# Kernel tuning notes

Measured on AMD Instinct MI355X. Metric: run time of the kernel, lower is better.

Reference implementation:

```python
import jax, jax.numpy as jnp
import numpy as np

B, M, D = 16, 16, 512          # m (tokens per sample) must equal num_experts
N = 16                          # num_experts
H = (D + D) * 2 // 3            # hidden_dim = 682
OUT = 512


def setup_inputs() -> dict:
    key = jax.random.key(0)
    ks = jax.random.split(key, 8)
    s = lambda k, shape, fan: jax.random.normal(k, shape, jnp.float32) / np.sqrt(fan)
    return {
        "x":    jax.random.normal(ks[0], (B, M, D), jnp.float32),
        "phi":  jax.random.normal(ks[1], (D, N, H), jnp.float32),
        "W1":   s(ks[2], (N, D, H), D),
        "b1":   s(ks[3], (N, H), D),
        "W2":   s(ks[4], (N, H, D), H),
        "b2":   s(ks[5], (N, D), H),
        "Wout": s(ks[6], (N * D, OUT), N * D),
        "bout": s(ks[7], (OUT,), N * D),
    }


def reference(x, phi, W1, b1, W2, b2, Wout, bout):
    # dispatch/combine logits: [b, m, n, p]
    logits = jnp.einsum('bmd,dnp->bmnp', x, phi)
    Dw = jax.nn.softmax(logits, axis=1)                       # dispatch weights over tokens m
    Cw = jax.nn.softmax(jax.nn.softmax(logits, axis=2), axis=3)  # (softmax of softmax, faithful)
    Xs = jnp.einsum('bmd,bmnp->bnpd', x, Dw)                  # expert slot inputs [b,n,p,d]
    # batched per-expert MLP (grouped GEMM over expert axis n)
    hmid = jax.nn.relu(jnp.einsum('bnpd,ndh->bnph', Xs, W1) + b1[None, :, None, :])
    Ys = jnp.einsum('bnph,nhd->bnpd', hmid, W2) + b2[None, :, None, :]
    Y = jnp.einsum('bnpd,bmnp->bmd', Ys, Cw)                  # combine -> [b, m, d]
    flat = Y.reshape(Y.shape[0], -1)                          # [b, m*d] == [b, n*d]
    return flat @ Wout + bout
```

## Files before the change

### kernel.cpp

```cpp
#include <hip/hip_runtime.h>
#include <hip/hip_bf16.h>
#include <math.h>

typedef unsigned int   u32;
typedef unsigned short u16;
typedef __bf16 bf16;
typedef bf16  bf16x8  __attribute__((ext_vector_type(8)));
typedef float f32x4   __attribute__((ext_vector_type(4)));
typedef float f32x16  __attribute__((ext_vector_type(16)));

#define BBATCH 16
#define MTOK   16
#define NEXP   16
#define DDIM   512
#define HDIM   682
#define HPAD   704
#define NHCOL  (NEXP*HDIM)
#define NHPCOL (NEXP*HPAD)

__device__ __forceinline__ u16 f2bf(float f) {
    u32 u = __builtin_bit_cast(u32, f);
    u += 0x7fffu + ((u >> 16) & 1u);
    return (u16)(u >> 16);
}
__device__ __forceinline__ float bf2f(u16 h) {
    u32 u = ((u32)h) << 16;
    return __builtin_bit_cast(float, u);
}
__device__ __forceinline__ u32 pk2bf(float a, float b) {
    __hip_bfloat162 t = __float22bfloat162_rn(float2{a, b});
    u32 r;
    __builtin_memcpy(&r, &t, 4);
    return r;
}

__global__ __launch_bounds__(256) void k_prep(
    const float* __restrict__ x,
    u16* __restrict__ xh, u16* __restrict__ xl) {
    const int bid = blockIdx.x, tid = threadIdx.x;
    int i = (bid * 256 + tid) * 4;
    float4 v = *(const float4*)&x[i];
    float a[4] = {v.x, v.y, v.z, v.w};
    u16 hh[4], ll[4];
    #pragma unroll
    for (int j = 0; j < 4; ++j) {
        hh[j] = f2bf(a[j]);
        ll[j] = f2bf(a[j] - bf2f(hh[j]));
    }
    *(uint2*)&xh[i] = make_uint2((u32)hh[0] | ((u32)hh[1] << 16), (u32)hh[2] | ((u32)hh[3] << 16));
    *(uint2*)&xl[i] = make_uint2((u32)ll[0] | ((u32)ll[1] << 16), (u32)ll[2] | ((u32)ll[3] << 16));
}

__global__ __launch_bounds__(256) void k_lt1(
    const u16* __restrict__ xh, const u16* __restrict__ xl,
    const float* __restrict__ phi, const float* __restrict__ W1,
    float* __restrict__ logits, u16* __restrict__ DwT, u16* __restrict__ T1b) {
    __shared__ __align__(16) char SMEM[29184];
    const int bid = blockIdx.x, tid = threadIdx.x;
    const int wv = tid >> 6, lane = tid & 63, quad = lane >> 4, l15 = lane & 15;
    if (bid < 704) {
        const int xcd = bid & 7, slot = bid >> 3;
        const int rt = slot & 3, ct = (slot >> 2) * 8 + xcd;
        if (ct >= 171) {
            const int hole = (slot & 3) * 5 + (xcd - 3);
            for (int g = hole * 256 + tid; g < 22528; g += 5120) {
                int bn = g / 88, off = g - bn * 88;
                *(uint2*)(DwT + (size_t)(bn * HPAD + HDIM) * 16 + off * 4) =
                    make_uint2(0u, 0u);
            }
            return;
        }
        u16* AH = (u16*)SMEM;
        u16* AL = (u16*)(SMEM + 5120);
        u16* BH = (u16*)(SMEM + 10240);
        u16* BL = (u16*)(SMEM + 15360);
        float* F = (float*)(SMEM + 20480);
        const int r = tid >> 2, kg = (tid & 3) * 8;
        const u16* aph = xh + (size_t)(rt * 64 + r) * 512 + kg;
        const u16* apl = xl + (size_t)(rt * 64 + r) * 512 + kg;
        const int dl = tid >> 3, cg = (tid & 7) * 8;
        const int c0 = ct * 64 + cg;
        float vB[8];
        auto loadB = [&](int kb) {
            const float* src = phi + (size_t)(kb + dl) * NHCOL + c0;
            if (c0 + 8 <= NHCOL) {
                *(float4*)&vB[0] = *(const float4*)&src[0];
                *(float4*)&vB[4] = *(const float4*)&src[4];
            } else {
                #pragma unroll
                for (int i = 0; i < 8; ++i) vB[i] = (c0 + i < NHCOL) ? src[i] : 0.f;
            }
        };
        uint4 rAh = *(const uint4*)aph;
        uint4 rAl = *(const uint4*)apl;
        loadB(0);
        f32x4 acc[4] = {};
        for (int kb = 0; kb < 512; kb += 32) {
            *(uint4*)&AH[r * 40 + kg] = rAh;
            *(uint4*)&AL[r * 40 + kg] = rAl;
            *(float4*)&F[dl * 68 + cg]     = *(float4*)&vB[0];
            *(float4*)&F[dl * 68 + cg + 4] = *(float4*)&vB[4];
            __syncthreads();
            if (kb + 32 < 512) {
                rAh = *(const uint4*)(aph + kb + 32);
                rAl = *(const uint4*)(apl + kb + 32);
                loadB(kb + 32);
            }
            {
                int cc = tid & 63, q = tid >> 6;
                u16 th[8], tl[8];
                #pragma unroll
                for (int i = 0; i < 8; ++i) {
                    float v = F[(q * 8 + i) * 68 + cc];
                    th[i] = f2bf(v);
                    tl[i] = f2bf(v - bf2f(th[i]));
                }
                *(uint4*)&BH[cc * 40 + q * 8] = *(uint4*)&th[0];
                *(uint4*)&BL[cc * 40 + q * 8] = *(uint4*)&tl[0];
            }
            __syncthreads();
            bf16x8 ah = *(const bf16x8*)&AH[(wv * 16 + l15) * 40 + quad * 8];
            bf16x8 al = *(const bf16x8*)&AL[(wv * 16 + l15) * 40 + quad * 8];
            #pragma unroll
            for (int j = 0; j < 4; ++j) {
                bf16x8 bh = *(const bf16x8*)&BH[(j * 16 + l15) * 40 + quad * 8];
                bf16x8 bl = *(const bf16x8*)&BL[(j * 16 + l15) * 40 + quad * 8];
                acc[j] = __builtin_amdgcn_mfma_f32_16x16x32_bf16(ah, bh, acc[j], 0, 0, 0);
                acc[j] = __builtin_amdgcn_mfma_f32_16x16x32_bf16(ah, bl, acc[j], 0, 0, 0);
                acc[j] = __builtin_amdgcn_mfma_f32_16x16x32_bf16(al, bh, acc[j], 0, 0, 0);
            }
            __syncthreads();
        }
        const int b  = rt * 4 + wv;
        const int r0 = rt * 64 + wv * 16 + quad * 4;
        #pragma unroll
        for (int j = 0; j < 4; ++j) {
            const int col = ct * 64 + j * 16 + l15;
            float a0 = acc[j][0], a1 = acc[j][1], a2 = acc[j][2], a3 = acc[j][3];
            if (col < NHCOL) {
                logits[(size_t)(r0 + 0) * NHCOL + col] = a0;
                logits[(size_t)(r0 + 1) * NHCOL + col] = a1;
                logits[(size_t)(r0 + 2) * NHCOL + col] = a2;
                logits[(size_t)(r0 + 3) * NHCOL + col] = a3;
            }
            float mx = fmaxf(fmaxf(a0, a1), fmaxf(a2, a3));
            mx = fmaxf(mx, __shfl_xor(mx, 16));
            mx = fmaxf(mx, __shfl_xor(mx, 32));
            float e0 = expf(a0 - mx), e1 = expf(a1 - mx);
            float e2 = expf(a2 - mx), e3 = expf(a3 - mx);
            float s = e0 + e1 + e2 + e3;
            s += __shfl_xor(s, 16);
            s += __shfl_xor(s, 32);
            float inv = 1.f / s;
            if (col < NHCOL) {
                int n = col / HDIM;
                int p2 = col - n * HDIM;
                u16* dst = DwT + ((size_t)((b * 16 + n) * HPAD + p2)) * 16 + quad * 4;
                *(uint2*)dst = make_uint2(pk2bf(e0 * inv, e1 * inv), pk2bf(e2 * inv, e3 * inv));
            }
        }
    } else {
        const int b2_ = bid - 704;
        const int xcd = b2_ & 7, slot = b2_ >> 3;
        const int rh = slot & 1, ct = (slot >> 1) * 8 + xcd;
        const int n = ct / 11, h0 = (ct % 11) * 64;
        u16* As = (u16*)SMEM;
        u16* Bs = (u16*)(SMEM + 10240);
        float* F = (float*)(SMEM + 15360);
        const int r = tid >> 1, kg = (tid & 1) * 16;
        const u16* ap = xh + (size_t)(rh * 128 + r) * 512 + kg;
        const int dl = tid >> 3, cg = (tid & 7) * 8;
        const int h = h0 + cg;
        float vB[8];
        auto loadB = [&](int kb) {
            const float* wr = W1 + ((size_t)n * 512 + kb + dl) * HDIM + h;
            if (h + 8 <= HDIM) {
                #pragma unroll
                for (int i = 0; i < 4; ++i) {
                    float2 t = *(const float2*)&wr[i * 2];
                    vB[i * 2] = t.x; vB[i * 2 + 1] = t.y;
                }
            } else {
                #pragma unroll
                for (int i = 0; i < 8; ++i) vB[i] = (h + i < HDIM) ? wr[i] : 0.f;
            }
        };
        uint4 rA0 = *(const uint4*)ap;
        uint4 rA1 = *(const uint4*)(ap + 8);
        loadB(0);
        f32x4 acc[2][4] = {};
        for (int kb = 0; kb < 512; kb += 32) {
            *(uint4*)&As[r * 40 + kg]     = rA0;
            *(uint4*)&As[r * 40 + kg + 8] = rA1;
            *(float4*)&F[dl * 68 + cg]     = *(float4*)&vB[0];
            *(float4*)&F[dl * 68 + cg + 4] = *(float4*)&vB[4];
            __syncthreads();
            if (kb + 32 < 512) {
                rA0 = *(const uint4*)(ap + kb + 32);
                rA1 = *(const uint4*)(ap + kb + 40);
                loadB(kb + 32);
            }
            {
                int cc = tid & 63, q = tid >> 6;
                u16 tv[8];
                #pragma unroll
                for (int i = 0; i < 8; ++i) tv[i] = f2bf(F[(q * 8 + i) * 68 + cc]);
                *(uint4*)&Bs[cc * 40 + q * 8] = *(uint4*)&tv[0];
            }
            __syncthreads();
            bf16x8 af[2], bfr[4];
            #pragma unroll
            for (int i = 0; i < 2; ++i)
                af[i] = *(const bf16x8*)&As[(wv * 32 + i * 16 + l15) * 40 + quad * 8];
            #pragma unroll
            for (int j = 0; j < 4; ++j)
                bfr[j] = *(const bf16x8*)&Bs[(j * 16 + l15) * 40 + quad * 8];
            #pragma unroll
            for (int i = 0; i < 2; ++i)
                #pragma unroll
                for (int j = 0; j < 4; ++j)
                    acc[i][j] = __builtin_amdgcn_mfma_f32_16x16x32_bf16(af[i], bfr[j], acc[i][j], 0, 0, 0);
            __syncthreads();
        }
        #pragma unroll
        for (int i = 0; i < 2; ++i)
            #pragma unroll
            for (int j = 0; j < 4; ++j) {
                int col = ct * 64 + j * 16 + l15;
                int r0  = rh * 128 + wv * 32 + i * 16 + quad * 4;
                #pragma unroll
                for (int rr = 0; rr < 4; ++rr)
                    T1b[(size_t)(r0 + rr) * NHPCOL + col] = f2bf(acc[i][j][rr]);
            }
    }
}

__global__ __launch_bounds__(512) void k_cw(
    const float* __restrict__ L, u16* __restrict__ CwB,
    const float* __restrict__ b2, const float* __restrict__ bout,
    float* __restrict__ Y, float* __restrict__ out) {
    __shared__ __align__(16) float row[NHCOL];
    const int bid = blockIdx.x, tid = threadIdx.x;
    if (bid >= 256) {
        if (bid < 512) {
            int idx = (bid - 256) * 512 + tid;
            int d = idx & 511;
            float s = 0.f;
            #pragma unroll
            for (int nn = 0; nn < 16; ++nn) s += b2[nn * 512 + d];
            Y[idx] = s;
        } else {
            int idx = (bid - 512) * 512 + tid;
            out[idx] = bout[idx & 511];
        }
        return;
    }
    const int m = bid & 15, b = bid >> 4;
    const float* Lrow = L + (size_t)(b * 16 + m) * NHCOL;
    for (int i4 = tid; i4 < NHCOL / 4; i4 += 512)
        *(float4*)&row[i4 * 4] = *(const float4*)&Lrow[i4 * 4];
    __syncthreads();
    for (int p = tid; p < HDIM; p += 512) {
        float v[16];
        float mx = -1e30f;
        #pragma unroll
        for (int n = 0; n < 16; ++n) { v[n] = row[n * HDIM + p]; mx = fmaxf(mx, v[n]); }
        float s = 0.f;
        #pragma unroll
        for (int n = 0; n < 16; ++n) { v[n] = expf(v[n] - mx); s += v[n]; }
        float inv = 1.f / s;
        #pragma unroll
        for (int n = 0; n < 16; ++n) row[n * HDIM + p] = expf(v[n] * inv);
    }
    __syncthreads();
    const int wv = tid >> 6, lane = tid & 63;
    for (int nn = 0; nn < 2; ++nn) {
        int n = wv * 2 + nn;
        float s = 0.f;
        for (int p = lane; p < HDIM; p += 64) s += row[n * HDIM + p];
        #pragma unroll
        for (int off = 32; off > 0; off >>= 1) s += __shfl_xor(s, off);
        float inv = 1.f / s;
        u16* dst = CwB + (size_t)(((b * 16 + n) * 16 + m)) * HPAD;
        for (int p = lane; p < HDIM; p += 64) dst[p] = f2bf(row[n * HDIM + p] * inv);
        if (lane < HPAD - HDIM) dst[HDIM + lane] = 0;
    }
}

__global__ __launch_bounds__(256) void k_mid(
    const u16* __restrict__ T1b, const u16* __restrict__ DwT,
    const u16* __restrict__ CwB, const float* __restrict__ b1,
    u16* __restrict__ Gb) {
    __shared__ u16 T1T[128 * 24];
    __shared__ u16 hmidT[128 * 64];
    const int bid = blockIdx.x;
    const int xcd = bid & 7, slot = bid >> 3;
    const int ht = slot % 6, gg = slot / 6;
    const int g = gg * 8 + xcd;
    const int n = g & 15, b = g >> 4;
    const int tid = threadIdx.x;
    const int wv = tid >> 6, lane = tid & 63;
    const int quad = lane >> 4, l15 = lane & 15;
    const int l31 = lane & 31, half = lane >> 5;
    const int h0 = ht * 128;
    const int b16n = b * 16 + n;

    {
        int m = tid & 15, hh0 = (tid >> 4) * 8;
        u16 v[8];
        if (h0 + hh0 + 8 <= HPAD) {
            *(uint4*)v = *(const uint4*)(T1b + (size_t)(b * 16 + m) * NHPCOL + n * HPAD + h0 + hh0);
        } else {
            #pragma unroll
            for (int i = 0; i < 8; ++i) v[i] = 0;
        }
        #pragma unroll
        for (int i = 0; i < 8; ++i) T1T[(hh0 + i) * 24 + m] = v[i];
    }
    __syncthreads();

    const int hrow = wv * 32 + l31;
    bf16x8 bt1 = *(const bf16x8*)&T1T[hrow * 24 + half * 8];
    int hg1 = h0 + hrow;
    float biasf = (hg1 < HDIM) ? b1[n * HDIM + hg1] : 0.f;
    f32x16 cbias;
    #pragma unroll
    for (int i = 0; i < 16; ++i) cbias[i] = biasf;

    const u16* dwbase = DwT + (size_t)(b16n * HPAD) * 16;
    const u16* cwrow  = CwB + (size_t)(b16n * 16 + l15) * HPAD;

    f32x4 acc[2] = {};
    const int hsw = hrow & 7;
    for (int c = 0; c < 11; ++c) {
        const int p0 = c * 64;
        #pragma unroll
        for (int pt = 0; pt < 2; ++pt) {
            bf16x8 adw = *(const bf16x8*)(dwbase + (size_t)(p0 + pt * 32 + l31) * 16 + half * 8);
            f32x16 hm = __builtin_amdgcn_mfma_f32_32x32x16_bf16(adw, bt1, cbias, 0, 0, 0);
            #pragma unroll
            for (int g2 = 0; g2 < 4; ++g2) {
                float v0 = fmaxf(hm[g2 * 4 + 0], 0.f);
                float v1 = fmaxf(hm[g2 * 4 + 1], 0.f);
                float v2 = fmaxf(hm[g2 * 4 + 2], 0.f);
                float v3 = fmaxf(hm[g2 * 4 + 3], 0.f);
                uint2 pk = make_uint2(pk2bf(v0, v1), pk2bf(v2, v3));
                int gran = (pt * 4 + g2) ^ hsw;
                *(uint2*)&hmidT[hrow * 64 + gran * 8 + half * 4] = pk;
            }
        }
        #pragma unroll
        for (int s = 0; s < 2; ++s) {
            bf16x8 acw = *(const bf16x8*)(cwrow + p0 + s * 32 + quad * 8);
            #pragma unroll
            for (int hj = 0; hj < 2; ++hj) {
                int hr = wv * 32 + hj * 16 + l15;
                int gr = (s * 4 + quad) ^ (hr & 7);
                bf16x8 bh = *(const bf16x8*)&hmidT[hr * 64 + gr * 8];
                acc[hj] = __builtin_amdgcn_mfma_f32_16x16x32_bf16(acw, bh, acc[hj], 0, 0, 0);
            }
        }
    }
    #pragma unroll
    for (int hj = 0; hj < 2; ++hj) {
        int h = h0 + wv * 32 + hj * 16 + l15;
        if (h < HPAD) {
            #pragma unroll
            for (int r = 0; r < 4; ++r) {
                int m = quad * 4 + r;
                Gb[(size_t)(b * 16 + m) * NHPCOL + n * HPAD + h] = f2bf(acc[hj][r]);
            }
        }
    }
}

__global__ __launch_bounds__(256) void k_ygemm(
    const u16* __restrict__ G, const float* __restrict__ W2, float* __restrict__ Y) {
    __shared__ u16 AsL[64 * 40];
    __shared__ u16 BsL[128 * 40];
    __shared__ float F[32 * 132];
    const int bid = blockIdx.x;
    const int xcd = bid & 7, slot = bid >> 3;
    const int rt = slot & 3, gg = slot >> 2;
    const int g = gg * 8 + xcd;
    const int ct = g & 3, nz = g >> 2;
    const int n = nz >> 1, kb0 = (nz & 1) * 352;
    const int tid = threadIdx.x;
    const int wv = tid >> 6, lane = tid & 63, quad = lane >> 4, l15 = lane & 15;
    const int m0 = rt * 64, d0 = ct * 128;
    const int am = tid >> 2, akg = (tid & 3) * 8;
    const u16* apg = G + (size_t)(m0 + am) * NHPCOL + n * HPAD + akg;
    const int hl = tid >> 3, cg = (tid & 7) * 16;
    float vB[16];
    auto loadB = [&](int kb) {
        int h = kb + hl;
        if (h < HDIM) {
            const float* src = W2 + ((size_t)n * HDIM + h) * 512 + d0 + cg;
            *(float4*)&vB[0]  = *(const float4*)&src[0];
            *(float4*)&vB[4]  = *(const float4*)&src[4];
            *(float4*)&vB[8]  = *(const float4*)&src[8];
            *(float4*)&vB[12] = *(const float4*)&src[12];
        } else {
            #pragma unroll
            for (int i = 0; i < 16; ++i) vB[i] = 0.f;
        }
    };
    uint4 rA = *(const uint4*)(apg + kb0);
    loadB(kb0);
    f32x4 acc[4][2] = {};
    for (int kb = kb0; kb < kb0 + 352; kb += 32) {
        *(uint4*)&AsL[am * 40 + akg] = rA;
        *(float4*)&F[hl * 132 + cg]      = *(float4*)&vB[0];
        *(float4*)&F[hl * 132 + cg + 4]  = *(float4*)&vB[4];
        *(float4*)&F[hl * 132 + cg + 8]  = *(float4*)&vB[8];
        *(float4*)&F[hl * 132 + cg + 12] = *(float4*)&vB[12];
        __syncthreads();
        if (kb + 32 < kb0 + 352) {
            rA = *(const uint4*)(apg + kb + 32);
            loadB(kb + 32);
        }
        {
            int cc = tid & 127, half = tid >> 7;
            u16 tv[16];
            #pragma unroll
            for (int i = 0; i < 16; ++i) tv[i] = f2bf(F[(half * 16 + i) * 132 + cc]);
            *(uint4*)&BsL[cc * 40 + half * 16]     = *(uint4*)&tv[0];
            *(uint4*)&BsL[cc * 40 + half * 16 + 8] = *(uint4*)&tv[8];
        }
        __syncthreads();
        bf16x8 af[4], bfr[2];
        #pragma unroll
        for (int i = 0; i < 4; ++i) af[i] = *(const bf16x8*)&AsL[(i * 16 + l15) * 40 + quad * 8];
        #pragma unroll
        for (int j = 0; j < 2; ++j) bfr[j] = *(const bf16x8*)&BsL[(wv * 32 + j * 16 + l15) * 40 + quad * 8];
        #pragma unroll
        for (int i = 0; i < 4; ++i)
            #pragma unroll
            for (int j = 0; j < 2; ++j)
                acc[i][j] = __builtin_amdgcn_mfma_f32_16x16x32_bf16(af[i], bfr[j], acc[i][j], 0, 0, 0);
        __syncthreads();
    }
    #pragma unroll
    for (int i = 0; i < 4; ++i)
        #pragma unroll
        for (int j = 0; j < 2; ++j) {
            int dcol = d0 + wv * 32 + j * 16 + l15;
            int r0 = m0 + i * 16 + quad * 4;
            #pragma unroll
            for (int r = 0; r < 4; ++r)
                atomicAdd(&Y[(size_t)(r0 + r) * 512 + dcol], acc[i][j][r]);
        }
}

__global__ __launch_bounds__(256) void k_outgemm(
    const float* __restrict__ Y, const float* __restrict__ Wout, float* __restrict__ out) {
    __shared__ u16 AsL[16 * 40];
    __shared__ u16 BsL[128 * 40];
    __shared__ float F[32 * 132];
    const int ct = blockIdx.x, ks = blockIdx.y;
    const int tid = threadIdx.x;
    const int wv = tid >> 6, lane = tid & 63, quad = lane >> 4, l15 = lane & 15;
    const int o0 = ct * 128, kbase = ks * 64;
    f32x4 acc[2] = {};
    for (int kb = 0; kb < 64; kb += 32) {
        {
            int r = tid >> 4, k2 = (tid & 15) * 2;
            float2 v = *(const float2*)&Y[(size_t)r * 8192 + kbase + kb + k2];
            AsL[r * 40 + k2]     = f2bf(v.x);
            AsL[r * 40 + k2 + 1] = f2bf(v.y);
        }
        {
            int kl = tid >> 3, cg = (tid & 7) * 16;
            const float* src = Wout + (size_t)(kbase + kb + kl) * 512 + o0 + cg;
            float v[16];
            *(float4*)&v[0]  = *(const float4*)&src[0];
            *(float4*)&v[4]  = *(const float4*)&src[4];
            *(float4*)&v[8]  = *(const float4*)&src[8];
            *(float4*)&v[12] = *(const float4*)&src[12];
            #pragma unroll
            for (int i = 0; i < 16; ++i) F[kl * 132 + cg + i] = v[i];
        }
        __syncthreads();
        {
            int cc = tid & 127, half = tid >> 7;
            u16 tv[16];
            #pragma unroll
            for (int i = 0; i < 16; ++i) tv[i] = f2bf(F[(half * 16 + i) * 132 + cc]);
            *(uint4*)&BsL[cc * 40 + half * 16]     = *(uint4*)&tv[0];
            *(uint4*)&BsL[cc * 40 + half * 16 + 8] = *(uint4*)&tv[8];
        }
        __syncthreads();
        bf16x8 af = *(const bf16x8*)&AsL[l15 * 40 + quad * 8];
        #pragma unroll
        for (int j = 0; j < 2; ++j) {
            bf16x8 bfr = *(const bf16x8*)&BsL[(wv * 32 + j * 16 + l15) * 40 + quad * 8];
            acc[j] = __builtin_amdgcn_mfma_f32_16x16x32_bf16(af, bfr, acc[j], 0, 0, 0);
        }
        __syncthreads();
    }
    #pragma unroll
    for (int j = 0; j < 2; ++j) {
        int o = o0 + wv * 32 + j * 16 + l15;
        #pragma unroll
        for (int r = 0; r < 4; ++r)
            atomicAdd(&out[(size_t)(quad * 4 + r) * 512 + o], acc[j][r]);
    }
}

extern "C" void kernel_launch(void* const* d_in, const int* in_sizes, int n_in,
                              void* d_out, int out_size, void* d_ws, size_t ws_size,
                              hipStream_t stream) {
    const float* x    = (const float*)d_in[0];
    const float* phi  = (const float*)d_in[1];
    const float* W1   = (const float*)d_in[2];
    const float* b1   = (const float*)d_in[3];
    const float* W2   = (const float*)d_in[4];
    const float* b2   = (const float*)d_in[5];
    const float* Wout = (const float*)d_in[6];
    const float* bout = (const float*)d_in[7];
    float* out = (float*)d_out;

    char* base = (char*)d_ws;
    float* logits = (float*)(base + 0);
    u16*   DwT    = (u16*)(base + 11173888);
    u16*   CwB    = (u16*)(base + 16941056);
    u16*   T1b    = (u16*)(base + 22708224);
    u16*   Gb     = (u16*)(base + 28475392);
    u16*   xh     = (u16*)(base + 34242560);
    u16*   xl     = (u16*)(base + 34504704);
    float* Y      = (float*)(base + 34766848);

    k_prep    <<<dim3(128), 256, 0, stream>>>(x, xh, xl);
    k_lt1     <<<dim3(1056), 256, 0, stream>>>(xh, xl, phi, W1, logits, DwT, T1b);
    k_cw      <<<dim3(528), 512, 0, stream>>>(logits, CwB, b2, bout, Y, out);
    k_mid     <<<dim3(1536), 256, 0, stream>>>(T1b, DwT, CwB, b1, Gb);
    k_ygemm   <<<dim3(512), 256, 0, stream>>>(Gb, W2, Y);
    k_outgemm <<<dim3(4, 128), 256, 0, stream>>>(Y, Wout, out);
}
```

Measured before the change: 209.0 us.

## Fuse mid stage with W2 GEMM, accumulating Y directly via atomics

Merges k_mid and k_ygemm into one kernel: each block stages its G tile (16 tokens x 128 hidden) in shared memory and multiplies it by the matching W2 slice, atomically adding partial results into Y. The Gb intermediate buffer and one kernel launch are removed, and the block-to-expert mapping is changed so each XCD keeps a fixed expert, which may help L2 reuse of W2. The cost is that W2 is read with scalar, strided global loads converted to bf16 per element with no shared-memory staging. Each W2 row is also read by all 16 batch blocks, and there are many more atomics into Y.

```diff
diff --git a/kernel.cpp b/kernel.cpp
--- a/kernel.cpp
+++ b/kernel.cpp
@@ -287,17 +287,19 @@
     }
 }
 
-__global__ __launch_bounds__(256) void k_mid(
+__global__ __launch_bounds__(256) void k_midy(
     const u16* __restrict__ T1b, const u16* __restrict__ DwT,
     const u16* __restrict__ CwB, const float* __restrict__ b1,
-    u16* __restrict__ Gb) {
-    __shared__ u16 T1T[128 * 24];
-    __shared__ u16 hmidT[128 * 64];
+    const float* __restrict__ W2, float* __restrict__ Y) {
+    __shared__ __align__(16) char SMEM[22528];
+    u16* T1T   = (u16*)SMEM;
+    u16* hmidT = (u16*)(SMEM + 6144);
+    u16* GT    = (u16*)SMEM;
     const int bid = blockIdx.x;
     const int xcd = bid & 7, slot = bid >> 3;
-    const int ht = slot % 6, gg = slot / 6;
-    const int g = gg * 8 + xcd;
-    const int n = g & 15, b = g >> 4;
+    const int nhi = slot & 1, rem = slot >> 1;
+    const int ht = rem % 6, b = rem / 6;
+    const int n = nhi * 8 + xcd;
     const int tid = threadIdx.x;
     const int wv = tid >> 6, lane = tid & 63;
     const int quad = lane >> 4, l15 = lane & 15;
@@ -361,95 +363,43 @@
             }
         }
     }
+
+    __syncthreads();
     #pragma unroll
     for (int hj = 0; hj < 2; ++hj) {
-        int h = h0 + wv * 32 + hj * 16 + l15;
-        if (h < HPAD) {
-            #pragma unroll
-            for (int r = 0; r < 4; ++r) {
-                int m = quad * 4 + r;
-                Gb[(size_t)(b * 16 + m) * NHPCOL + n * HPAD + h] = f2bf(acc[hj][r]);
-            }
-        }
-    }
-}
-
-__global__ __launch_bounds__(256) void k_ygemm(
-    const u16* __restrict__ G, const float* __restrict__ W2, float* __restrict__ Y) {
-    __shared__ u16 AsL[64 * 40];
-    __shared__ u16 BsL[128 * 40];
-    __shared__ float F[32 * 132];
-    const int bid = blockIdx.x;
-    const int xcd = bid & 7, slot = bid >> 3;
-    const int rt = slot & 3, gg = slot >> 2;
-    const int g = gg * 8 + xcd;
-    const int ct = g & 3, nz = g >> 2;
-    const int n = nz >> 1, kb0 = (nz & 1) * 352;
-    const int tid = threadIdx.x;
-    const int wv = tid >> 6, lane = tid & 63, quad = lane >> 4, l15 = lane & 15;
-    const int m0 = rt * 64, d0 = ct * 128;
-    const int am = tid >> 2, akg = (tid & 3) * 8;
-    const u16* apg = G + (size_t)(m0 + am) * NHPCOL + n * HPAD + akg;
-    const int hl = tid >> 3, cg = (tid & 7) * 16;
-    float vB[16];
-    auto loadB = [&](int kb) {
-        int h = kb + hl;
-        if (h < HDIM) {
-            const float* src = W2 + ((size_t)n * HDIM + h) * 512 + d0 + cg;
-            *(float4*)&vB[0]  = *(const float4*)&src[0];
-            *(float4*)&vB[4]  = *(const float4*)&src[4];
-            *(float4*)&vB[8]  = *(const float4*)&src[8];
-            *(float4*)&vB[12] = *(const float4*)&src[12];
-        } else {
-            #pragma unroll
-            for (int i = 0; i < 16; ++i) vB[i] = 0.f;
-        }
-    };
-    uint4 rA = *(const uint4*)(apg + kb0);
-    loadB(kb0);
-    f32x4 acc[4][2] = {};
-    for (int kb = kb0; kb < kb0 + 352; kb += 32) {
-        *(uint4*)&AsL[am * 40 + akg] = rA;
-        *(float4*)&F[hl * 132 + cg]      = *(float4*)&vB[0];
-        *(float4*)&F[hl * 132 + cg + 4]  = *(float4*)&vB[4];
-        *(float4*)&F[hl * 132 + cg + 8]  = *(float4*)&vB[8];
-        *(float4*)&F[hl * 132 + cg + 12] = *(float4*)&vB[12];
-        __syncthreads();
-        if (kb + 32 < kb0 + 352) {
-            rA = *(const uint4*)(apg + kb + 32);
-            loadB(kb + 32);
-        }
-        {
-            int cc = tid & 127, half = tid >> 7;
-            u16 tv[16];
-            #pragma unroll
-            for (int i = 0; i < 16; ++i) tv[i] = f2bf(F[(half * 16 + i) * 132 + cc]);
-            *(uint4*)&BsL[cc * 40 + half * 16]     = *(uint4*)&tv[0];
-            *(uint4*)&BsL[cc * 40 + half * 16 + 8] = *(uint4*)&tv[8];
-        }
-        __syncthreads();
-        bf16x8 af[4], bfr[2];
-        #pragma unroll
-        for (int i = 0; i < 4; ++i) af[i] = *(const bf16x8*)&AsL[(i * 16 + l15) * 40 + quad * 8];
-        #pragma unroll
-        for (int j = 0; j < 2; ++j) bfr[j] = *(const bf16x8*)&BsL[(wv * 32 + j * 16 + l15) * 40 + quad * 8];
-        #pragma unroll
-        for (int i = 0; i < 4; ++i)
-            #pragma unroll
-            for (int j = 0; j < 2; ++j)
-                acc[i][j] = __builtin_amdgcn_mfma_f32_16x16x32_bf16(af[i], bfr[j], acc[i][j], 0, 0, 0);
-        __syncthreads();
-    }
-    #pragma unroll
-    for (int i = 0; i < 4; ++i)
-        #pragma unroll
-        for (int j = 0; j < 2; ++j) {
-            int dcol = d0 + wv * 32 + j * 16 + l15;
-            int r0 = m0 + i * 16 + quad * 4;
-            #pragma unroll
-            for (int r = 0; r < 4; ++r)
-                atomicAdd(&Y[(size_t)(r0 + r) * 512 + dcol], acc[i][j][r]);
-        }
+        int lh = wv * 32 + hj * 16 + l15;
+        #pragma unroll
+        for (int r = 0; r < 4; ++r)
+            GT[(quad * 4 + r) * 136 + lh] = f2bf(acc[hj][r]);
+    }
+    __syncthreads();
+
+    const int dbase = wv * 128;
+    f32x4 acc2[8] = {};
+    #pragma unroll
+    for (int q = 0; q < 4; ++q) {
+        bf16x8 ga = *(const bf16x8*)&GT[l15 * 136 + q * 32 + quad * 8];
+        #pragma unroll
+        for (int dt = 0; dt < 8; ++dt) {
+            const int dcol = dbase + dt * 16 + l15;
+            u16 bb[8];
+            #pragma unroll
+            for (int i = 0; i < 8; ++i) {
+                int hh = h0 + q * 32 + quad * 8 + i;
+                float w = (hh < HDIM) ? W2[((size_t)n * HDIM + hh) * 512 + dcol] : 0.f;
+                bb[i] = f2bf(w);
+            }
+            acc2[dt] = __builtin_amdgcn_mfma_f32_16x16x32_bf16(
+                ga, *(const bf16x8*)&bb[0], acc2[dt], 0, 0, 0);
+        }
+    }
+    #pragma unroll
+    for (int dt = 0; dt < 8; ++dt) {
+        const int dcol = dbase + dt * 16 + l15;
+        #pragma unroll
+        for (int r = 0; r < 4; ++r)
+            atomicAdd(&Y[(size_t)(b * 16 + quad * 4 + r) * 512 + dcol], acc2[dt][r]);
+    }
 }
 
 __global__ __launch_bounds__(256) void k_outgemm(
@@ -525,7 +475,6 @@
     u16*   DwT    = (u16*)(base + 11173888);
     u16*   CwB    = (u16*)(base + 16941056);
     u16*   T1b    = (u16*)(base + 22708224);
-    u16*   Gb     = (u16*)(base + 28475392);
     u16*   xh     = (u16*)(base + 34242560);
     u16*   xl     = (u16*)(base + 34504704);
     float* Y      = (float*)(base + 34766848);
@@ -533,7 +482,6 @@
     k_prep    <<<dim3(128), 256, 0, stream>>>(x, xh, xl);
     k_lt1     <<<dim3(1056), 256, 0, stream>>>(xh, xl, phi, W1, logits, DwT, T1b);
     k_cw      <<<dim3(528), 512, 0, stream>>>(logits, CwB, b2, bout, Y, out);
-    k_mid     <<<dim3(1536), 256, 0, stream>>>(T1b, DwT, CwB, b1, Gb);
-    k_ygemm   <<<dim3(512), 256, 0, stream>>>(Gb, W2, Y);
+    k_midy    <<<dim3(1536), 256, 0, stream>>>(T1b, DwT, CwB, b1, W2, Y);
     k_outgemm <<<dim3(4, 128), 256, 0, stream>>>(Y, Wout, out);
 }
```

After: 231.8 us. 1.11x slower.
